# Kernel tuning notes

Hardware: AMD Instinct MI355X
Metric: run time of the kernel (lower is better)

## Reference

```python
import jax, jax.numpy as jnp
import numpy as np

N = 50000      # nodes per type
E = 600000     # edges per relation
D_IN = 128
D_OUT = 64


def setup_inputs() -> dict:
    key = jax.random.key(0)
    ks = jax.random.split(key, 12)
    x_v0 = jax.random.normal(ks[0], (N, D_IN), dtype=jnp.float32)
    x_v1 = jax.random.normal(ks[1], (N, D_IN), dtype=jnp.float32)
    edge_v0 = jax.random.randint(ks[2], (2, E), 0, N, dtype=jnp.int64)
    edge_v1 = jax.random.randint(ks[3], (2, E), 0, N, dtype=jnp.int64)
    s = 1.0 / np.sqrt(D_IN)
    Wrel0 = jax.random.uniform(ks[4], (D_OUT, D_IN), jnp.float32, -s, s)
    brel0 = jax.random.uniform(ks[5], (D_OUT,), jnp.float32, -s, s)
    Wroot0 = jax.random.uniform(ks[6], (D_OUT, D_IN), jnp.float32, -s, s)
    Wrel1 = jax.random.uniform(ks[7], (D_OUT, D_IN), jnp.float32, -s, s)
    brel1 = jax.random.uniform(ks[8], (D_OUT,), jnp.float32, -s, s)
    Wroot1 = jax.random.uniform(ks[9], (D_OUT, D_IN), jnp.float32, -s, s)
    sf = 1.0 / np.sqrt(2 * D_OUT)
    Wfc = jax.random.uniform(ks[10], (1, 2 * D_OUT), jnp.float32, -sf, sf)
    bfc = jax.random.uniform(ks[11], (1,), jnp.float32, -sf, sf)
    return {"x_v0": x_v0, "x_v1": x_v1, "edge_v0": edge_v0, "edge_v1": edge_v1,
            "Wrel0": Wrel0, "brel0": brel0, "Wroot0": Wroot0,
            "Wrel1": Wrel1, "brel1": brel1, "Wroot1": Wroot1,
            "Wfc": Wfc, "bfc": bfc}


def _graph_conv(x, edge_index, Wrel, brel, Wroot):
    # PyG GraphConv (aggr='add'): out = lin_rel(sum_{j in N(i)} x_j) + lin_root(x_i)
    src, dst = edge_index[0], edge_index[1]
    agg = jax.ops.segment_sum(x[src], dst, num_segments=x.shape[0])  # [N, D_IN]
    return agg @ Wrel.T + brel + x @ Wroot.T


def reference(x_v0, x_v1, edge_v0, edge_v1, Wrel0, brel0, Wroot0,
              Wrel1, brel1, Wroot1, Wfc, bfc):
    h0 = jax.nn.relu(_graph_conv(x_v0, edge_v0, Wrel0, brel0, Wroot0))  # [N, 64]
    h1 = jax.nn.relu(_graph_conv(x_v1, edge_v1, Wrel1, brel1, Wroot1))  # [N, 64]
    h = jnp.concatenate([h0, h1], axis=1)  # [N, 128]
    return h @ Wfc.T + bfc  # [N, 1]
```

## Files before the change

kernel.cpp:

```cpp
#include <hip/hip_runtime.h>
#include <hip/hip_bf16.h>

typedef __attribute__((ext_vector_type(8))) short short8;
typedef __attribute__((ext_vector_type(4))) float floatx4;

#define NB    1000
#define BPN   50
#define BCAP  832
#define CHUNK 2048

static __device__ __forceinline__ unsigned short bf16_of(float f) {
    union { float f; unsigned u; } v; v.f = f;
    unsigned r = (v.u + 0x7FFF + ((v.u >> 16) & 1)) >> 16;
    return (unsigned short)r;
}
static __device__ __forceinline__ float f32_of(unsigned short b) {
    union { float f; unsigned u; } v; v.u = ((unsigned)b) << 16;
    return v.f;
}

__global__ __launch_bounds__(256) void convert_w(
    const float* __restrict__ Wrel0, const float* __restrict__ Wroot0,
    const float* __restrict__ Wrel1, const float* __restrict__ Wroot1,
    unsigned short* __restrict__ Wb0, unsigned short* __restrict__ Wb1)
{
    int c = blockIdx.x * 256 + threadIdx.x;
    if (c >= 4096) return;
    const float* s; unsigned short* d;
    if      (c < 1024) { s = Wrel0 + c * 8;           d = Wb0 + c * 8; }
    else if (c < 2048) { int t = c - 1024; s = Wroot0 + t * 8; d = Wb0 + 8192 + t * 8; }
    else if (c < 3072) { int t = c - 2048; s = Wrel1 + t * 8;  d = Wb1 + t * 8; }
    else               { int t = c - 3072; s = Wroot1 + t * 8; d = Wb1 + 8192 + t * 8; }

    floatx4 v0 = *(const floatx4*)s;
    floatx4 v1 = *(const floatx4*)(s + 4);
    short8 r = { (short)bf16_of(v0[0]), (short)bf16_of(v0[1]),
                 (short)bf16_of(v0[2]), (short)bf16_of(v0[3]),
                 (short)bf16_of(v1[0]), (short)bf16_of(v1[1]),
                 (short)bf16_of(v1[2]), (short)bf16_of(v1[3]) };
    *(short8*)d = r;
}

__global__ __launch_bounds__(256) void gemm_mfma(
    const float* __restrict__ X0, const float* __restrict__ X1,
    const unsigned short* __restrict__ Wb0, const unsigned short* __restrict__ Wb1,
    unsigned short* __restrict__ Y0, unsigned short* __restrict__ Y1, int N)
{
    const float* X           = blockIdx.y ? X1 : X0;
    const unsigned short* Wb = blockIdx.y ? Wb1 : Wb0;
    unsigned short* Y        = blockIdx.y ? Y1 : Y0;

    __shared__ __align__(16) short x_sh[32 * 136];
    __shared__ __align__(16) short w_sh[128 * 136];

    const int tid = threadIdx.x;
    const int m0  = blockIdx.x * 32;

#pragma unroll
    for (int i = 0; i < 8; ++i) {
        int c   = tid + 256 * i;
        int row = c >> 4;
        int kc  = (c & 15) * 8;
        *(short8*)&w_sh[row * 136 + kc] = *(const short8*)(Wb + row * 128 + kc);
    }
#pragma unroll
    for (int i = 0; i < 4; ++i) {
        int c    = tid + 256 * i;
        int row  = c >> 5;
        int f    = (c & 31) * 4;
        int node = m0 + row;
        floatx4 v = {};
        if (node < N) v = *(const floatx4*)(X + (size_t)node * 128 + f);
        short* d = &x_sh[row * 136 + f];
        d[0] = (short)bf16_of(v[0]); d[1] = (short)bf16_of(v[1]);
        d[2] = (short)bf16_of(v[2]); d[3] = (short)bf16_of(v[3]);
    }
    __syncthreads();

    const int w    = tid >> 6;
    const int lane = tid & 63;
    const int q    = lane >> 4;
    const int r    = lane & 15;

    floatx4 acc[2][2] = {};
#pragma unroll
    for (int ko = 0; ko < 4; ++ko) {
        int kb = ko * 32 + q * 8;
        short8 a0 = *(const short8*)&x_sh[(r) * 136 + kb];
        short8 a1 = *(const short8*)&x_sh[(16 + r) * 136 + kb];
        short8 b0 = *(const short8*)&w_sh[(w * 32 + r) * 136 + kb];
        short8 b1 = *(const short8*)&w_sh[(w * 32 + 16 + r) * 136 + kb];
        acc[0][0] = __builtin_amdgcn_mfma_f32_16x16x32_bf16(a0, b0, acc[0][0], 0, 0, 0);
        acc[0][1] = __builtin_amdgcn_mfma_f32_16x16x32_bf16(a0, b1, acc[0][1], 0, 0, 0);
        acc[1][0] = __builtin_amdgcn_mfma_f32_16x16x32_bf16(a1, b0, acc[1][0], 0, 0, 0);
        acc[1][1] = __builtin_amdgcn_mfma_f32_16x16x32_bf16(a1, b1, acc[1][1], 0, 0, 0);
    }

#pragma unroll
    for (int mt = 0; mt < 2; ++mt)
#pragma unroll
        for (int nt = 0; nt < 2; ++nt) {
            int col = w * 32 + nt * 16 + r;
#pragma unroll
            for (int reg = 0; reg < 4; ++reg) {
                int node = m0 + mt * 16 + q * 4 + reg;
                if (node < N)
                    Y[(size_t)node * 128 + col] = bf16_of(acc[mt][nt][reg]);
            }
        }
}

__global__ __launch_bounds__(256) void bucket_pass(
    const int* __restrict__ e0, const int* __restrict__ e1,
    unsigned int* __restrict__ pairs0, unsigned int* __restrict__ pairs1,
    int* __restrict__ cur0, int* __restrict__ cur1, int E, int N)
{
    const int* e        = blockIdx.y ? e1 : e0;
    unsigned int* pairs = blockIdx.y ? pairs1 : pairs0;
    int* cur            = blockIdx.y ? cur1 : cur0;

    __shared__ unsigned int   stage[CHUNK];
    __shared__ unsigned short sbuck[CHUNK];
    __shared__ int hist[NB];
    __shared__ int loff[NB];
    __shared__ int lcur[NB];
    __shared__ int gbase[NB];
    __shared__ int scanb[256];

    const int tid = threadIdx.x;
    const int c0  = blockIdx.x * CHUNK;
    const int n   = min(CHUNK, E - c0);

    for (int b = tid; b < NB; b += 256) hist[b] = 0;
    __syncthreads();

#pragma unroll
    for (int k = 0; k < CHUNK / 256; ++k) {
        int i = c0 + k * 256 + tid;
        if (i < c0 + n) {
            int dst = e[E + i];
            if ((unsigned)dst < (unsigned)N)
                atomicAdd(&hist[(unsigned)dst / BPN], 1);
        }
    }
    __syncthreads();

    int t4 = tid * 4, v[4], s = 0;
#pragma unroll
    for (int k = 0; k < 4; ++k) {
        int b = t4 + k;
        v[k] = (b < NB) ? hist[b] : 0;
        s += v[k];
    }
    scanb[tid] = s;
    __syncthreads();
    for (int off = 1; off < 256; off <<= 1) {
        int x = (tid >= off) ? scanb[tid - off] : 0;
        __syncthreads();
        scanb[tid] += x;
        __syncthreads();
    }
    int run = scanb[tid] - s;
#pragma unroll
    for (int k = 0; k < 4; ++k) {
        int b = t4 + k;
        if (b < NB) { loff[b] = run; lcur[b] = run; }
        run += v[k];
    }
    for (int b = tid; b < NB; b += 256)
        gbase[b] = (hist[b] > 0) ? atomicAdd(&cur[b], hist[b]) : 0;
    __syncthreads();

#pragma unroll
    for (int k = 0; k < CHUNK / 256; ++k) {
        int i = c0 + k * 256 + tid;
        if (i < c0 + n) {
            int src = e[i];
            int dst = e[E + i];
            if ((unsigned)dst < (unsigned)N) {
                unsigned usrc = ((unsigned)src < (unsigned)N) ? (unsigned)src : 0u;
                int b = (unsigned)dst / BPN;
                int p = atomicAdd(&lcur[b], 1);
                stage[p] = ((unsigned)dst << 16) | usrc;
                sbuck[p] = (unsigned short)b;
            }
        }
    }
    __syncthreads();

    int total = scanb[255];
    for (int p = tid; p < total; p += 256) {
        int b = sbuck[p];
        int g = gbase[b] + (p - loff[b]);
        if (g < BCAP)
            pairs[(size_t)b * BCAP + g] = stage[p];
    }
}

__global__ __launch_bounds__(512) void bucket_gather(
    const unsigned int* __restrict__ pairs0, const unsigned int* __restrict__ pairs1,
    const int* __restrict__ cur0, const int* __restrict__ cur1,
    const unsigned short* __restrict__ Y0, const unsigned short* __restrict__ Y1,
    const float* __restrict__ brel0, const float* __restrict__ brel1,
    const float* __restrict__ wfc, const float* __restrict__ bfc,
    float* __restrict__ out, int N)
{
    __shared__ unsigned short slist0[BCAP], slist1[BCAP];
    __shared__ int cnt0s[BPN], cnt1s[BPN];
    __shared__ int off0s[BPN], off1s[BPN];
    __shared__ int cur0s[BPN], cur1s[BPN];

    const int tid  = threadIdx.x;
    const int b    = blockIdx.x;
    const int wv   = tid >> 6;
    const int lane = tid & 63;

    for (int i = tid; i < BPN; i += 512) { cnt0s[i] = 0; cnt1s[i] = 0; }
    __syncthreads();

    const int n0 = min(cur0[b], BCAP);
    const int n1 = min(cur1[b], BCAP);
    const unsigned base = (unsigned)(b * BPN);

    for (int j = tid; j < n0; j += 512)
        atomicAdd(&cnt0s[(pairs0[(size_t)b * BCAP + j] >> 16) - base], 1);
    for (int j = tid; j < n1; j += 512)
        atomicAdd(&cnt1s[(pairs1[(size_t)b * BCAP + j] >> 16) - base], 1);
    __syncthreads();

    if (wv == 0) {
        int c = (lane < BPN) ? cnt0s[lane] : 0;
        int inc = c;
#pragma unroll
        for (int d = 1; d < 64; d <<= 1) {
            int t = __shfl_up(inc, d, 64);
            if (lane >= d) inc += t;
        }
        if (lane < BPN) { off0s[lane] = inc - c; cur0s[lane] = inc - c; }
    } else if (wv == 1) {
        int c = (lane < BPN) ? cnt1s[lane] : 0;
        int inc = c;
#pragma unroll
        for (int d = 1; d < 64; d <<= 1) {
            int t = __shfl_up(inc, d, 64);
            if (lane >= d) inc += t;
        }
        if (lane < BPN) { off1s[lane] = inc - c; cur1s[lane] = inc - c; }
    }
    __syncthreads();

    for (int j = tid; j < n0; j += 512) {
        unsigned p = pairs0[(size_t)b * BCAP + j];
        int pos = atomicAdd(&cur0s[(p >> 16) - base], 1);
        slist0[pos] = (unsigned short)(p & 0xFFFFu);
    }
    for (int j = tid; j < n1; j += 512) {
        unsigned p = pairs1[(size_t)b * BCAP + j];
        int pos = atomicAdd(&cur1s[(p >> 16) - base], 1);
        slist1[pos] = (unsigned short)(p & 0xFFFFu);
    }
    __syncthreads();

    const float br0 = brel0[lane], br1 = brel1[lane];
    const float w0  = wfc[lane],   w1  = wfc[64 + lane];
    const float bias = bfc[0];

    for (int nl = wv; nl < BPN; nl += 8) {
        int i = b * BPN + nl;
        float a0 = 0.f, a1 = 0.f;
        {
            int st = off0s[nl], d = cnt0s[nl], j = 0;
            for (; j + 3 < d; j += 4) {
                int s0 = slist0[st + j], s1 = slist0[st + j + 1];
                int s2 = slist0[st + j + 2], s3 = slist0[st + j + 3];
                float v0 = f32_of(Y0[(size_t)s0 * 128 + lane]);
                float v1 = f32_of(Y0[(size_t)s1 * 128 + lane]);
                float v2 = f32_of(Y0[(size_t)s2 * 128 + lane]);
                float v3 = f32_of(Y0[(size_t)s3 * 128 + lane]);
                a0 += (v0 + v1) + (v2 + v3);
            }
            for (; j < d; ++j)
                a0 += f32_of(Y0[(size_t)slist0[st + j] * 128 + lane]);
        }
        {
            int st = off1s[nl], d = cnt1s[nl], j = 0;
            for (; j + 3 < d; j += 4) {
                int s0 = slist1[st + j], s1 = slist1[st + j + 1];
                int s2 = slist1[st + j + 2], s3 = slist1[st + j + 3];
                float v0 = f32_of(Y1[(size_t)s0 * 128 + lane]);
                float v1 = f32_of(Y1[(size_t)s1 * 128 + lane]);
                float v2 = f32_of(Y1[(size_t)s2 * 128 + lane]);
                float v3 = f32_of(Y1[(size_t)s3 * 128 + lane]);
                a1 += (v0 + v1) + (v2 + v3);
            }
            for (; j < d; ++j)
                a1 += f32_of(Y1[(size_t)slist1[st + j] * 128 + lane]);
        }
        float h0 = fmaxf(a0 + br0 + f32_of(Y0[(size_t)i * 128 + 64 + lane]), 0.f);
        float h1 = fmaxf(a1 + br1 + f32_of(Y1[(size_t)i * 128 + 64 + lane]), 0.f);
        float s = h0 * w0 + h1 * w1;
#pragma unroll
        for (int m = 32; m > 0; m >>= 1) s += __shfl_xor(s, m, 64);
        if (lane == 0) out[i] = s + bias;
    }
}

extern "C" void kernel_launch(void* const* d_in, const int* in_sizes, int n_in,
                              void* d_out, int out_size, void* d_ws, size_t ws_size,
                              hipStream_t stream)
{
    const int N = in_sizes[0] / 128;
    const int E = in_sizes[2] / 2;

    const float* x0     = (const float*)d_in[0];
    const float* x1     = (const float*)d_in[1];
    const int*   e0     = (const int*)d_in[2];
    const int*   e1     = (const int*)d_in[3];
    const float* Wrel0  = (const float*)d_in[4];
    const float* brel0  = (const float*)d_in[5];
    const float* Wroot0 = (const float*)d_in[6];
    const float* Wrel1  = (const float*)d_in[7];
    const float* brel1  = (const float*)d_in[8];
    const float* Wroot1 = (const float*)d_in[9];
    const float* wfc    = (const float*)d_in[10];
    const float* bfc    = (const float*)d_in[11];
    float* out = (float*)d_out;

    unsigned short* Wb0 = (unsigned short*)d_ws;
    unsigned short* Wb1 = Wb0 + 128 * 128;
    unsigned short* Y0  = Wb1 + 128 * 128;
    unsigned short* Y1  = Y0 + (size_t)N * 128;
    unsigned int* pairs0 = (unsigned int*)(Y1 + (size_t)N * 128);
    unsigned int* pairs1 = pairs0 + (size_t)NB * BCAP;
    int* cur0 = (int*)(pairs1 + (size_t)NB * BCAP);
    int* cur1 = cur0 + NB;

    (void)hipMemsetAsync(cur0, 0, 2 * NB * sizeof(int), stream);

    convert_w<<<16, 256, 0, stream>>>(Wrel0, Wroot0, Wrel1, Wroot1, Wb0, Wb1);

    dim3 gemm_grid((N + 31) / 32, 2);
    gemm_mfma<<<gemm_grid, 256, 0, stream>>>(x0, x1, Wb0, Wb1, Y0, Y1, N);

    dim3 bp_grid((E + CHUNK - 1) / CHUNK, 2);
    bucket_pass<<<bp_grid, 256, 0, stream>>>(e0, e1, pairs0, pairs1,
                                             cur0, cur1, E, N);

    bucket_gather<<<NB, 512, 0, stream>>>(pairs0, pairs1, cur0, cur1, Y0, Y1,
                                          brel0, brel1, wfc, bfc, out, N);
}
```

Baseline: 187.5 us.

## Split rel/root GEMM outputs into compact arrays and gather two edges per wave

The projected features are now stored as separate dense N×64 bf16 arrays for the rel and root parts instead of one interleaved N×128 array, so each gathered neighbour row is a contiguous 128-byte line. The gather wave splits into two halves that each read a different edge with 32-bit loads holding two bf16 values, and a cross-half shuffle combines them. This aims to halve wasted cache-line traffic and double memory-level parallelism in the random gather. The GEMM tile also grows to 128 rows per block with each wave covering all columns, which uses more LDS per block and may reduce occupancy.

After: 193.1 us. 3.0% more time.

```diff
diff --git a/kernel.cpp b/kernel.cpp
--- a/kernel.cpp
+++ b/kernel.cpp
@@ -14,9 +14,11 @@
     unsigned r = (v.u + 0x7FFF + ((v.u >> 16) & 1)) >> 16;
     return (unsigned short)r;
 }
-static __device__ __forceinline__ float f32_of(unsigned short b) {
-    union { float f; unsigned u; } v; v.u = ((unsigned)b) << 16;
-    return v.f;
+static __device__ __forceinline__ float lo_f(unsigned u) {
+    union { float f; unsigned u; } v; v.u = u << 16; return v.f;
+}
+static __device__ __forceinline__ float hi_f(unsigned u) {
+    union { float f; unsigned u; } v; v.u = u & 0xFFFF0000u; return v.f;
 }
 
 __global__ __launch_bounds__(256) void convert_w(
@@ -44,17 +46,20 @@
 __global__ __launch_bounds__(256) void gemm_mfma(
     const float* __restrict__ X0, const float* __restrict__ X1,
     const unsigned short* __restrict__ Wb0, const unsigned short* __restrict__ Wb1,
-    unsigned short* __restrict__ Y0, unsigned short* __restrict__ Y1, int N)
+    unsigned short* __restrict__ Yrel0, unsigned short* __restrict__ Yrel1,
+    unsigned short* __restrict__ Yroot0, unsigned short* __restrict__ Yroot1,
+    int N)
 {
     const float* X           = blockIdx.y ? X1 : X0;
     const unsigned short* Wb = blockIdx.y ? Wb1 : Wb0;
-    unsigned short* Y        = blockIdx.y ? Y1 : Y0;
-
-    __shared__ __align__(16) short x_sh[32 * 136];
+    unsigned short* Yrel     = blockIdx.y ? Yrel1 : Yrel0;
+    unsigned short* Yroot    = blockIdx.y ? Yroot1 : Yroot0;
+
+    __shared__ __align__(16) short x_sh[128 * 136];
     __shared__ __align__(16) short w_sh[128 * 136];
 
     const int tid = threadIdx.x;
-    const int m0  = blockIdx.x * 32;
+    const int m0  = blockIdx.x * 128;
 
 #pragma unroll
     for (int i = 0; i < 8; ++i) {
@@ -64,7 +69,7 @@
         *(short8*)&w_sh[row * 136 + kc] = *(const short8*)(Wb + row * 128 + kc);
     }
 #pragma unroll
-    for (int i = 0; i < 4; ++i) {
+    for (int i = 0; i < 16; ++i) {
         int c    = tid + 256 * i;
         int row  = c >> 5;
         int f    = (c & 31) * 4;
@@ -77,35 +82,37 @@
     }
     __syncthreads();
 
-    const int w    = tid >> 6;
+    const int wv   = tid >> 6;
     const int lane = tid & 63;
     const int q    = lane >> 4;
     const int r    = lane & 15;
 
-    floatx4 acc[2][2] = {};
+    floatx4 acc[2][8] = {};
 #pragma unroll
     for (int ko = 0; ko < 4; ++ko) {
         int kb = ko * 32 + q * 8;
-        short8 a0 = *(const short8*)&x_sh[(r) * 136 + kb];
-        short8 a1 = *(const short8*)&x_sh[(16 + r) * 136 + kb];
-        short8 b0 = *(const short8*)&w_sh[(w * 32 + r) * 136 + kb];
-        short8 b1 = *(const short8*)&w_sh[(w * 32 + 16 + r) * 136 + kb];
-        acc[0][0] = __builtin_amdgcn_mfma_f32_16x16x32_bf16(a0, b0, acc[0][0], 0, 0, 0);
-        acc[0][1] = __builtin_amdgcn_mfma_f32_16x16x32_bf16(a0, b1, acc[0][1], 0, 0, 0);
-        acc[1][0] = __builtin_amdgcn_mfma_f32_16x16x32_bf16(a1, b0, acc[1][0], 0, 0, 0);
-        acc[1][1] = __builtin_amdgcn_mfma_f32_16x16x32_bf16(a1, b1, acc[1][1], 0, 0, 0);
+        short8 a0 = *(const short8*)&x_sh[(wv * 32 + r) * 136 + kb];
+        short8 a1 = *(const short8*)&x_sh[(wv * 32 + 16 + r) * 136 + kb];
+#pragma unroll
+        for (int nt = 0; nt < 8; ++nt) {
+            short8 b = *(const short8*)&w_sh[(nt * 16 + r) * 136 + kb];
+            acc[0][nt] = __builtin_amdgcn_mfma_f32_16x16x32_bf16(a0, b, acc[0][nt], 0, 0, 0);
+            acc[1][nt] = __builtin_amdgcn_mfma_f32_16x16x32_bf16(a1, b, acc[1][nt], 0, 0, 0);
+        }
     }
 
 #pragma unroll
     for (int mt = 0; mt < 2; ++mt)
 #pragma unroll
-        for (int nt = 0; nt < 2; ++nt) {
-            int col = w * 32 + nt * 16 + r;
+        for (int nt = 0; nt < 8; ++nt) {
+            int col = nt * 16 + r;
 #pragma unroll
             for (int reg = 0; reg < 4; ++reg) {
-                int node = m0 + mt * 16 + q * 4 + reg;
-                if (node < N)
-                    Y[(size_t)node * 128 + col] = bf16_of(acc[mt][nt][reg]);
+                int row = m0 + wv * 32 + mt * 16 + q * 4 + reg;
+                if (row < N) {
+                    if (nt < 4) Yrel[(size_t)row * 64 + col] = bf16_of(acc[mt][nt][reg]);
+                    else        Yroot[(size_t)row * 64 + (col - 64)] = bf16_of(acc[mt][nt][reg]);
+                }
             }
         }
 }
@@ -200,7 +207,8 @@
 __global__ __launch_bounds__(512) void bucket_gather(
     const unsigned int* __restrict__ pairs0, const unsigned int* __restrict__ pairs1,
     const int* __restrict__ cur0, const int* __restrict__ cur1,
-    const unsigned short* __restrict__ Y0, const unsigned short* __restrict__ Y1,
+    const unsigned short* __restrict__ Yrel0, const unsigned short* __restrict__ Yrel1,
+    const unsigned short* __restrict__ Yroot0, const unsigned short* __restrict__ Yroot1,
     const float* __restrict__ brel0, const float* __restrict__ brel1,
     const float* __restrict__ wfc, const float* __restrict__ bfc,
     float* __restrict__ out, int N)
@@ -214,6 +222,8 @@
     const int b    = blockIdx.x;
     const int wv   = tid >> 6;
     const int lane = tid & 63;
+    const int c    = lane & 31;
+    const int half = lane >> 5;
 
     for (int i = tid; i < BPN; i += 512) { cnt0s[i] = 0; cnt1s[i] = 0; }
     __syncthreads();
@@ -229,23 +239,23 @@
     __syncthreads();
 
     if (wv == 0) {
-        int c = (lane < BPN) ? cnt0s[lane] : 0;
-        int inc = c;
+        int cc = (lane < BPN) ? cnt0s[lane] : 0;
+        int inc = cc;
 #pragma unroll
         for (int d = 1; d < 64; d <<= 1) {
             int t = __shfl_up(inc, d, 64);
             if (lane >= d) inc += t;
         }
-        if (lane < BPN) { off0s[lane] = inc - c; cur0s[lane] = inc - c; }
+        if (lane < BPN) { off0s[lane] = inc - cc; cur0s[lane] = inc - cc; }
     } else if (wv == 1) {
-        int c = (lane < BPN) ? cnt1s[lane] : 0;
-        int inc = c;
+        int cc = (lane < BPN) ? cnt1s[lane] : 0;
+        int inc = cc;
 #pragma unroll
         for (int d = 1; d < 64; d <<= 1) {
             int t = __shfl_up(inc, d, 64);
             if (lane >= d) inc += t;
         }
-        if (lane < BPN) { off1s[lane] = inc - c; cur1s[lane] = inc - c; }
+        if (lane < BPN) { off1s[lane] = inc - cc; cur1s[lane] = inc - cc; }
     }
     __syncthreads();
 
@@ -261,46 +271,75 @@
     }
     __syncthreads();
 
-    const float br0 = brel0[lane], br1 = brel1[lane];
-    const float w0  = wfc[lane],   w1  = wfc[64 + lane];
+    const float2 br0 = ((const float2*)brel0)[c];
+    const float2 br1 = ((const float2*)brel1)[c];
+    const float2 w0  = ((const float2*)wfc)[c];
+    const float2 w1  = ((const float2*)(wfc + 64))[c];
     const float bias = bfc[0];
 
     for (int nl = wv; nl < BPN; nl += 8) {
         int i = b * BPN + nl;
-        float a0 = 0.f, a1 = 0.f;
+        float a0x = 0.f, a0y = 0.f, a1x = 0.f, a1y = 0.f;
+
         {
             int st = off0s[nl], d = cnt0s[nl], j = 0;
-            for (; j + 3 < d; j += 4) {
-                int s0 = slist0[st + j], s1 = slist0[st + j + 1];
-                int s2 = slist0[st + j + 2], s3 = slist0[st + j + 3];
-                float v0 = f32_of(Y0[(size_t)s0 * 128 + lane]);
-                float v1 = f32_of(Y0[(size_t)s1 * 128 + lane]);
-                float v2 = f32_of(Y0[(size_t)s2 * 128 + lane]);
-                float v3 = f32_of(Y0[(size_t)s3 * 128 + lane]);
-                a0 += (v0 + v1) + (v2 + v3);
-            }
-            for (; j < d; ++j)
-                a0 += f32_of(Y0[(size_t)slist0[st + j] * 128 + lane]);
+            for (; j + 7 < d; j += 8) {
+                int i0 = slist0[st + j + half];
+                int i1 = slist0[st + j + 2 + half];
+                int i2 = slist0[st + j + 4 + half];
+                int i3 = slist0[st + j + 6 + half];
+                unsigned u0 = ((const unsigned*)(Yrel0 + ((size_t)i0 << 6)))[c];
+                unsigned u1 = ((const unsigned*)(Yrel0 + ((size_t)i1 << 6)))[c];
+                unsigned u2 = ((const unsigned*)(Yrel0 + ((size_t)i2 << 6)))[c];
+                unsigned u3 = ((const unsigned*)(Yrel0 + ((size_t)i3 << 6)))[c];
+                a0x += (lo_f(u0) + lo_f(u1)) + (lo_f(u2) + lo_f(u3));
+                a0y += (hi_f(u0) + hi_f(u1)) + (hi_f(u2) + hi_f(u3));
+            }
+            for (; j < d; j += 2) {
+                int jj = j + half;
+                int idx = slist0[st + (jj < d ? jj : d - 1)];
+                unsigned u = ((const unsigned*)(Yrel0 + ((size_t)idx << 6)))[c];
+                if (jj < d) { a0x += lo_f(u); a0y += hi_f(u); }
+            }
         }
         {
             int st = off1s[nl], d = cnt1s[nl], j = 0;
-            for (; j + 3 < d; j += 4) {
-                int s0 = slist1[st + j], s1 = slist1[st + j + 1];
-                int s2 = slist1[st + j + 2], s3 = slist1[st + j + 3];
-                float v0 = f32_of(Y1[(size_t)s0 * 128 + lane]);
-                float v1 = f32_of(Y1[(size_t)s1 * 128 + lane]);
-                float v2 = f32_of(Y1[(size_t)s2 * 128 + lane]);
-                float v3 = f32_of(Y1[(size_t)s3 * 128 + lane]);
-                a1 += (v0 + v1) + (v2 + v3);
-            }
-            for (; j < d; ++j)
-                a1 += f32_of(Y1[(size_t)slist1[st + j] * 128 + lane]);
-        }
-        float h0 = fmaxf(a0 + br0 + f32_of(Y0[(size_t)i * 128 + 64 + lane]), 0.f);
-        float h1 = fmaxf(a1 + br1 + f32_of(Y1[(size_t)i * 128 + 64 + lane]), 0.f);
-        float s = h0 * w0 + h1 * w1;
-#pragma unroll
-        for (int m = 32; m > 0; m >>= 1) s += __shfl_xor(s, m, 64);
+            for (; j + 7 < d; j += 8) {
+                int i0 = slist1[st + j + half];
+                int i1 = slist1[st + j + 2 + half];
+                int i2 = slist1[st + j + 4 + half];
+                int i3 = slist1[st + j + 6 + half];
+                unsigned u0 = ((const unsigned*)(Yrel1 + ((size_t)i0 << 6)))[c];
+                unsigned u1 = ((const unsigned*)(Yrel1 + ((size_t)i1 << 6)))[c];
+                unsigned u2 = ((const unsigned*)(Yrel1 + ((size_t)i2 << 6)))[c];
+                unsigned u3 = ((const unsigned*)(Yrel1 + ((size_t)i3 << 6)))[c];
+                a1x += (lo_f(u0) + lo_f(u1)) + (lo_f(u2) + lo_f(u3));
+                a1y += (hi_f(u0) + hi_f(u1)) + (hi_f(u2) + hi_f(u3));
+            }
+            for (; j < d; j += 2) {
+                int jj = j + half;
+                int idx = slist1[st + (jj < d ? jj : d - 1)];
+                unsigned u = ((const unsigned*)(Yrel1 + ((size_t)idx << 6)))[c];
+                if (jj < d) { a1x += lo_f(u); a1y += hi_f(u); }
+            }
+        }
+
+        a0x += __shfl_xor(a0x, 32, 64);
+        a0y += __shfl_xor(a0y, 32, 64);
+        a1x += __shfl_xor(a1x, 32, 64);
+        a1y += __shfl_xor(a1y, 32, 64);
+
+        unsigned ur0 = ((const unsigned*)(Yroot0 + ((size_t)i << 6)))[c];
+        unsigned ur1 = ((const unsigned*)(Yroot1 + ((size_t)i << 6)))[c];
+
+        float h0x = fmaxf(a0x + br0.x + lo_f(ur0), 0.f);
+        float h0y = fmaxf(a0y + br0.y + hi_f(ur0), 0.f);
+        float h1x = fmaxf(a1x + br1.x + lo_f(ur1), 0.f);
+        float h1y = fmaxf(a1y + br1.y + hi_f(ur1), 0.f);
+        float s = h0x * w0.x + h0y * w0.y + h1x * w1.x + h1y * w1.y;
+
+#pragma unroll
+        for (int m = 16; m > 0; m >>= 1) s += __shfl_xor(s, m, 64);
         if (lane == 0) out[i] = s + bias;
     }
 }
@@ -326,11 +365,13 @@
     const float* bfc    = (const float*)d_in[11];
     float* out = (float*)d_out;
 
-    unsigned short* Wb0 = (unsigned short*)d_ws;
-    unsigned short* Wb1 = Wb0 + 128 * 128;
-    unsigned short* Y0  = Wb1 + 128 * 128;
-    unsigned short* Y1  = Y0 + (size_t)N * 128;
-    unsigned int* pairs0 = (unsigned int*)(Y1 + (size_t)N * 128);
+    unsigned short* Wb0   = (unsigned short*)d_ws;
+    unsigned short* Wb1   = Wb0 + 128 * 128;
+    unsigned short* Yrel0 = Wb1 + 128 * 128;
+    unsigned short* Yrel1 = Yrel0 + (size_t)N * 64;
+    unsigned short* Yroot0 = Yrel1 + (size_t)N * 64;
+    unsigned short* Yroot1 = Yroot0 + (size_t)N * 64;
+    unsigned int* pairs0 = (unsigned int*)(Yroot1 + (size_t)N * 64);
     unsigned int* pairs1 = pairs0 + (size_t)NB * BCAP;
     int* cur0 = (int*)(pairs1 + (size_t)NB * BCAP);
     int* cur1 = cur0 + NB;
@@ -339,13 +380,15 @@
 
     convert_w<<<16, 256, 0, stream>>>(Wrel0, Wroot0, Wrel1, Wroot1, Wb0, Wb1);
 
-    dim3 gemm_grid((N + 31) / 32, 2);
-    gemm_mfma<<<gemm_grid, 256, 0, stream>>>(x0, x1, Wb0, Wb1, Y0, Y1, N);
+    dim3 gemm_grid((N + 127) / 128, 2);
+    gemm_mfma<<<gemm_grid, 256, 0, stream>>>(x0, x1, Wb0, Wb1,
+                                             Yrel0, Yrel1, Yroot0, Yroot1, N);
 
     dim3 bp_grid((E + CHUNK - 1) / CHUNK, 2);
     bucket_pass<<<bp_grid, 256, 0, stream>>>(e0, e1, pairs0, pairs1,
                                              cur0, cur1, E, N);
 
-    bucket_gather<<<NB, 512, 0, stream>>>(pairs0, pairs1, cur0, cur1, Y0, Y1,
+    bucket_gather<<<NB, 512, 0, stream>>>(pairs0, pairs1, cur0, cur1,
+                                          Yrel0, Yrel1, Yroot0, Yroot1,
                                           brel0, brel1, wfc, bfc, out, N);
 }
```
